# Kernel optimization log

Measured on AMD Instinct MI355X. Metric: run time of the kernel, lower is better.

The kernel has to match this reference:

```python
import jax, jax.numpy as jnp
import numpy as np

B, S, D = 2, 2048, 2048
H, KVH, HD = 16, 4, 128
E, TOPK, F = 8, 2, 1024
EPS = 1e-6
THETA = 10000.0


def _rmsnorm(x, w):
    return x * jax.lax.rsqrt(jnp.mean(x * x, axis=-1, keepdims=True) + EPS) * w


def _rope(x):
    # x: [B, S, h, HD]; positions 0..S-1 (prefill, pos offset 0)
    half = HD // 2
    inv_freq = THETA ** (-jnp.arange(half, dtype=jnp.float32) / half)  # [half]
    ang = jnp.arange(S, dtype=jnp.float32)[:, None] * inv_freq  # [S, half]
    cos = jnp.cos(ang)[None, :, None, :]
    sin = jnp.sin(ang)[None, :, None, :]
    x1, x2 = x[..., :half], x[..., half:]
    return jnp.concatenate([x1 * cos - x2 * sin, x1 * sin + x2 * cos], axis=-1)


def setup_inputs() -> dict:
    key = jax.random.key(0)
    ks = jax.random.split(key, 16)
    sc = 0.02
    return {
        "x": jax.random.normal(ks[0], (B, S, D), jnp.float32),
        "wattn_norm": 1.0 + 0.1 * jax.random.normal(ks[1], (D,), jnp.float32),
        "wq": sc * jax.random.normal(ks[2], (H * HD, D), jnp.float32),
        "wk": sc * jax.random.normal(ks[3], (KVH * HD, D), jnp.float32),
        "wv": sc * jax.random.normal(ks[4], (KVH * HD, D), jnp.float32),
        "wq_norm": 1.0 + 0.1 * jax.random.normal(ks[5], (HD,), jnp.float32),
        "wk_norm": 1.0 + 0.1 * jax.random.normal(ks[6], (HD,), jnp.float32),
        "wattn_out": sc * jax.random.normal(ks[7], (D, H * HD), jnp.float32),
        "wffn_norm": 1.0 + 0.1 * jax.random.normal(ks[8], (D,), jnp.float32),
        "w_router": sc * jax.random.normal(ks[9], (E, D), jnp.float32),
        "w_gate": sc * jax.random.normal(ks[10], (E, F, D), jnp.float32),
        "w_up": sc * jax.random.normal(ks[11], (E, F, D), jnp.float32),
        "w_down": sc * jax.random.normal(ks[12], (E, D, F), jnp.float32),
    }


def reference(x, wattn_norm, wq, wk, wv, wq_norm, wk_norm, wattn_out,
              wffn_norm, w_router, w_gate, w_up, w_down):
    # ---- attention sub-block ----
    h = _rmsnorm(x, wattn_norm)
    q = (h @ wq.T).reshape(B, S, H, HD)
    k = (h @ wk.T).reshape(B, S, KVH, HD)
    v = (h @ wv.T).reshape(B, S, KVH, HD)
    # per-head q/k rmsnorm (attn_q_norm / attn_k_norm)
    q = _rmsnorm(q, wq_norm)
    k = _rmsnorm(k, wk_norm)
    q = _rope(q)
    k = _rope(k)
    # GQA: repeat kv heads
    rep = H // KVH
    k = jnp.repeat(k, rep, axis=2)  # [B,S,H,HD]
    v = jnp.repeat(v, rep, axis=2)
    scores = jnp.einsum("bqhd,bkhd->bhqk", q, k) / np.sqrt(HD)
    causal = jnp.tril(jnp.ones((S, S), dtype=bool))
    scores = jnp.where(causal[None, None], scores, jnp.finfo(scores.dtype).min)
    attn = jax.nn.softmax(scores, axis=-1)
    o = jnp.einsum("bhqk,bkhd->bqhd", attn, v).reshape(B, S, H * HD)
    x = x + o @ wattn_out.T

    # ---- MoE FFN sub-block ----
    h = _rmsnorm(x, wffn_norm)  # [B,S,D]
    logits = h @ w_router.T  # [B,S,E]
    probs = jax.nn.softmax(logits, axis=-1)
    topv, topi = jax.lax.top_k(probs, TOPK)  # [B,S,K]
    topv = topv / jnp.sum(topv, axis=-1, keepdims=True)
    gates = jnp.sum(jax.nn.one_hot(topi, E, dtype=h.dtype) * topv[..., None], axis=-2)  # [B,S,E]

    t = h.reshape(B * S, D)
    g = gates.reshape(B * S, E)
    gh = jnp.einsum("td,efd->tef", t, w_gate)
    uh = jnp.einsum("td,efd->tef", t, w_up)
    act = jax.nn.silu(gh) * uh  # [T,E,F]
    eo = jnp.einsum("tef,edf->ted", act, w_down)  # [T,E,D]
    y = jnp.einsum("ted,te->td", eo, g).reshape(B, S, D)
    return x + y
```

## Files before the change

### kernel.cpp

```cpp
#include <hip/hip_runtime.h>

typedef _Float16 f16;
typedef __attribute__((ext_vector_type(8))) _Float16 f16x8;
typedef __attribute__((ext_vector_type(4))) _Float16 f16x4;
typedef __attribute__((ext_vector_type(4))) float f32x4;


#define GLD_LDS(gp, lp) \
  __builtin_amdgcn_global_load_lds((__attribute__((address_space(1))) void*)(gp), \
                                   (__attribute__((address_space(3))) void*)(lp), 16, 0, 0)


__global__ __launch_bounds__(256) void cvt_f16(const float* __restrict__ in,
                                               f16* __restrict__ outp, int n4) {
  int i = blockIdx.x * 256 + threadIdx.x;
  if (i >= n4) return;
  float4 v = ((const float4*)in)[i];
  f16x4 o;
  o[0] = (f16)v.x; o[1] = (f16)v.y; o[2] = (f16)v.z; o[3] = (f16)v.w;
  ((f16x4*)outp)[i] = o;
}

__global__ __launch_bounds__(256) void cvt_gu(const float* __restrict__ in,
                                              f16* __restrict__ outp, int up) {
  int i4 = blockIdx.x * 256 + threadIdx.x;
  int e = i4 >> 19;
  float4 v = ((const float4*)in)[i4];
  f16x4 o;
  o[0] = (f16)v.x; o[1] = (f16)v.y; o[2] = (f16)v.z; o[3] = (f16)v.w;
  ((f16x4*)outp)[i4 + (long)(e + up) * 524288] = o;
}

__global__ __launch_bounds__(256) void rope_tables(float* __restrict__ cost,
                                                   float* __restrict__ sint) {
  int i = blockIdx.x * 256 + threadIdx.x;
  if (i >= 2048 * 64) return;
  int s = i >> 6, j = i & 63;
  float invf = powf(10000.f, -(float)j * (1.f / 64.f));
  float ang = (float)s * invf;
  cost[i] = cosf(ang);
  sint[i] = sinf(ang);
}

__global__ __launch_bounds__(256) void rmsnorm_f16(const float* __restrict__ X,
                                                   const float* __restrict__ w,
                                                   f16* __restrict__ outp) {
  int t = blockIdx.x, tid = threadIdx.x;
  const float* row = X + (long)t * 2048;
  float4 v0 = ((const float4*)row)[tid];
  float4 v1 = ((const float4*)row)[tid + 256];
  float ss = v0.x * v0.x + v0.y * v0.y + v0.z * v0.z + v0.w * v0.w +
             v1.x * v1.x + v1.y * v1.y + v1.z * v1.z + v1.w * v1.w;
  for (int o = 32; o; o >>= 1) ss += __shfl_xor(ss, o);
  __shared__ float red[4];
  if ((tid & 63) == 0) red[tid >> 6] = ss;
  __syncthreads();
  ss = red[0] + red[1] + red[2] + red[3];
  float inv = rsqrtf(ss * (1.f / 2048.f) + 1e-6f);
  float4 w0 = ((const float4*)w)[tid];
  float4 w1 = ((const float4*)w)[tid + 256];
  f16x4 a, b;
  a[0] = (f16)(v0.x * inv * w0.x); a[1] = (f16)(v0.y * inv * w0.y);
  a[2] = (f16)(v0.z * inv * w0.z); a[3] = (f16)(v0.w * inv * w0.w);
  b[0] = (f16)(v1.x * inv * w1.x); b[1] = (f16)(v1.y * inv * w1.y);
  b[2] = (f16)(v1.z * inv * w1.z); b[3] = (f16)(v1.w * inv * w1.w);
  f16x4* orow = (f16x4*)(outp + (long)t * 2048);
  orow[tid] = a;
  orow[tid + 256] = b;
}

__global__ __launch_bounds__(256) void gemm_nt(
    const f16* __restrict__ A, const f16* __restrict__ W0,
    float* __restrict__ C, const float* __restrict__ Res, f16* __restrict__ Ct,
    f16* __restrict__ Ch,
    const int* __restrict__ gather, const int* __restrict__ eoff,
    const int* __restrict__ ecnt, int M, int N, int K, long wstride) {
  int e = blockIdx.z;
  int row0 = 0, nrows = M;
  if (eoff) { row0 = eoff[e]; nrows = ecnt[e]; }
  int mt = blockIdx.x;
  if (mt * 128 >= nrows) return;
  int nt = blockIdx.y;
  const f16* W = W0 + (long)e * wstride;

  __shared__ __align__(16) f16 As[128 * 64];
  __shared__ __align__(16) f16 Bs[128 * 64];

  int tid = threadIdx.x;
  int lane = tid & 63, wid = tid >> 6;
  int quad = lane >> 4, l15 = lane & 15;
  int wm = wid & 1, wn = wid >> 1;

  int srow = tid >> 3, ssub = tid & 7;
  long arowK[4], browK[4];
  for (int r = 0; r < 4; r++) {
    int rw = r * 32 + srow;
    int lr = mt * 128 + rw;
    int g = (lr < nrows) ? (row0 + lr) : row0;
    arowK[r] = (long)(gather ? gather[g] : g) * K;
    browK[r] = (long)(nt * 128 + rw) * K;
  }
  int gcol = ((ssub ^ (srow & 7)) * 8);

  f32x4 acc[4][4] = {};
  for (int k0 = 0; k0 < K; k0 += 64) {
    __syncthreads();
    for (int r = 0; r < 4; r++) {
      GLD_LDS(A + arowK[r] + k0 + gcol, &As[(r * 256 + tid) * 8]);
      GLD_LDS(W + browK[r] + k0 + gcol, &Bs[(r * 256 + tid) * 8]);
    }
    __syncthreads();
    for (int c = 0; c < 2; c++) {
      f16x8 av[4], bv[4];
      for (int i = 0; i < 4; i++) {
        int row = wm * 64 + i * 16 + l15;
        av[i] = *(const f16x8*)&As[row * 64 + (((c * 4 + quad) ^ (row & 7)) * 8)];
      }
      for (int j = 0; j < 4; j++) {
        int row = wn * 64 + j * 16 + l15;
        bv[j] = *(const f16x8*)&Bs[row * 64 + (((c * 4 + quad) ^ (row & 7)) * 8)];
      }
      for (int i = 0; i < 4; i++)
        for (int j = 0; j < 4; j++)
          acc[i][j] = __builtin_amdgcn_mfma_f32_16x16x32_f16(av[i], bv[j], acc[i][j], 0, 0, 0);
    }
  }
  for (int i = 0; i < 4; i++) {
    int lrb = mt * 128 + wm * 64 + i * 16 + quad * 4;
    for (int rr = 0; rr < 4; rr++) {
      int lr = lrb + rr;
      if (lr >= nrows) continue;
      long orow = row0 + lr;
      if (Ct) {
        int bb = (int)(orow >> 11), s2 = (int)(orow & 2047);
        for (int j = 0; j < 4; j++) {
          int col = nt * 128 + wn * 64 + j * 16 + l15;
          Ct[((long)(bb * N + col)) * 2048 + s2] = (f16)acc[i][j][rr];
        }
      } else if (Ch) {
        for (int j = 0; j < 4; j++) {
          int col = nt * 128 + wn * 64 + j * 16 + l15;
          Ch[orow * N + col] = (f16)acc[i][j][rr];
        }
      } else {
        for (int j = 0; j < 4; j++) {
          int col = nt * 128 + wn * 64 + j * 16 + l15;
          float v = acc[i][j][rr];
          if (Res) v += Res[orow * N + col];
          C[orow * N + col] = v;
        }
      }
    }
  }
}

__global__ __launch_bounds__(256) void qknorm_rope(
    const f16* __restrict__ X, const float* __restrict__ wn,
    const float* __restrict__ cost, const float* __restrict__ sint,
    f16* __restrict__ outp, int nh, float scale) {
  int t = blockIdx.x;
  int b = t >> 11, s = t & 2047;
  int wv = threadIdx.x >> 6, ln = threadIdx.x & 63;
  float c = cost[s * 64 + ln], sn = sint[s * 64 + ln];
  float w1 = wn[ln], w2 = wn[ln + 64];
  for (int h = wv; h < nh; h += 4) {
    const f16* row = X + ((long)t * nh + h) * 128;
    float x1 = (float)row[ln], x2 = (float)row[ln + 64];
    float ss = x1 * x1 + x2 * x2;
    for (int o = 32; o; o >>= 1) ss += __shfl_xor(ss, o);
    float inv = rsqrtf(ss * (1.f / 128.f) + 1e-6f);
    float n1 = x1 * inv * w1, n2 = x2 * inv * w2;
    f16* orow = outp + ((long)(b * nh + h) * 2048 + s) * 128;
    orow[ln] = (f16)((n1 * c - n2 * sn) * scale);
    orow[ln + 64] = (f16)((n1 * sn + n2 * c) * scale);
  }
}

__global__ __launch_bounds__(256, 3) void attn_kernel(
    const f16* __restrict__ Q, const f16* __restrict__ Kb,
    const f16* __restrict__ Vtg, f16* __restrict__ O) {
  int jj = blockIdx.x;
  int bh = blockIdx.y;
  int b = bh >> 4, h = bh & 15;
  int kvh = h >> 2;
  int tid = threadIdx.x, lane = tid & 63, wid = tid >> 6;
  int quad = lane >> 4, l15 = lane & 15;

  const f16* Kg = Kb + (long)(b * 4 + kvh) * 2048 * 128;
  const f16* Vg = Vtg + (long)(b * 4 + kvh) * 128 * 2048;

  const int KSTR = 136, VSTR = 72, PSTR = 72;
  __shared__ __align__(16) f16 Ks[64 * 136];
  __shared__ __align__(16) f16 Vs[128 * 72];
  __shared__ __align__(16) f16 Ps[4][16 * 72];

  int krow[4], kc[4], vd[4], vc[4];
  for (int c2 = 0; c2 < 4; c2++) {
    int idx = c2 * 256 + tid;
    krow[c2] = idx >> 4; kc[c2] = (idx & 15) * 8;
    vd[c2] = idx >> 3;  vc[c2] = (idx & 7) * 8;
  }

  for (int ph = 0; ph < 2; ph++) {
    int qt = ph ? (31 - jj) : jj;
    int q0 = qt * 64;
    int rowb = q0 + wid * 16 + quad * 4;

    const f16* Qb = Q + ((long)(b * 16 + h) * 2048 + q0 + wid * 16) * 128;
    f16x8 qfr[4];
    for (int c = 0; c < 4; c++)
      qfr[c] = *(const f16x8*)(Qb + (long)l15 * 128 + c * 32 + quad * 8);

    f32x4 oacc[8] = {};
    float li[4] = {0.f, 0.f, 0.f, 0.f};

    f16x8 kpre[4], vpre[4];
    for (int c2 = 0; c2 < 4; c2++) {
      kpre[c2] = *(const f16x8*)(Kg + (long)krow[c2] * 128 + kc[c2]);
      vpre[c2] = *(const f16x8*)(Vg + (long)vd[c2] * 2048 + vc[c2]);
    }

    for (int kt = 0; kt <= qt; kt++) {
      int k0 = kt * 64;
      __syncthreads();
      for (int c2 = 0; c2 < 4; c2++) {
        *(f16x8*)&Ks[krow[c2] * KSTR + kc[c2]] = kpre[c2];
        *(f16x8*)&Vs[vd[c2] * VSTR + vc[c2]] = vpre[c2];
      }
      if (kt < qt) {
        int k1 = (kt + 1) * 64;
        for (int c2 = 0; c2 < 4; c2++) {
          kpre[c2] = *(const f16x8*)(Kg + (long)(k1 + krow[c2]) * 128 + kc[c2]);
          vpre[c2] = *(const f16x8*)(Vg + (long)vd[c2] * 2048 + k1 + vc[c2]);
        }
      }
      __syncthreads();
      f32x4 sc[4] = {};
      for (int hf = 0; hf < 4; hf++)
        for (int c = 0; c < 4; c++) {
          f16x8 kf = *(const f16x8*)&Ks[(hf * 16 + l15) * KSTR + c * 32 + quad * 8];
          sc[hf] = __builtin_amdgcn_mfma_f32_16x16x32_f16(qfr[c], kf, sc[hf], 0, 0, 0);
        }
      bool dg = (kt == qt);
      for (int r = 0; r < 4; r++) {
        int row = rowb + r;
        float acc = 0.f;
        for (int hf = 0; hf < 4; hf++) {
          float pv = exp2f(sc[hf][r] * 1.44269504f - 7.21347520f);
          if (dg && (k0 + hf * 16 + l15 > row)) pv = 0.f;
          f16 phh = (f16)pv;
          Ps[wid][(quad * 4 + r) * PSTR + hf * 16 + l15] = phh;
          acc += (float)phh;
        }
        li[r] += acc;
      }
      for (int c = 0; c < 2; c++) {
        f16x8 pa = *(const f16x8*)&Ps[wid][l15 * PSTR + c * 32 + quad * 8];
        for (int n = 0; n < 8; n++) {
          f16x8 vf = *(const f16x8*)&Vs[(n * 16 + l15) * VSTR + c * 32 + quad * 8];
          oacc[n] = __builtin_amdgcn_mfma_f32_16x16x32_f16(pa, vf, oacc[n], 0, 0, 0);
        }
      }
    }
    for (int r = 0; r < 4; r++) {
      float s = li[r];
      for (int o = 8; o; o >>= 1) s += __shfl_xor(s, o);
      float inv = 1.f / s;
      int row = rowb + r;
      long basep = ((long)(b * 2048 + row)) * 2048 + h * 128;
      for (int n = 0; n < 8; n++)
        O[basep + n * 16 + l15] = (f16)(oacc[n][r] * inv);
    }
  }
}

__global__ void zero8(int* p) { if (threadIdx.x < 8) p[threadIdx.x] = 0; }

__global__ __launch_bounds__(256) void router_kernel(
    const float* __restrict__ X2, const float* __restrict__ wfn,
    const float* __restrict__ wr, int* __restrict__ route,
    int* __restrict__ toke, float* __restrict__ tokw) {
  int t = blockIdx.x, tid = threadIdx.x;
  const float* row = X2 + (long)t * 2048;
  float xv[8];
  float ss = 0.f;
  for (int j = 0; j < 8; j++) {
    float v = row[tid + j * 256];
    xv[j] = v;
    ss += v * v;
  }
  for (int o = 32; o; o >>= 1) ss += __shfl_xor(ss, o);
  __shared__ float red[4];
  int lane = tid & 63, wid = tid >> 6;
  if (lane == 0) red[wid] = ss;
  __syncthreads();
  ss = red[0] + red[1] + red[2] + red[3];
  float inv = rsqrtf(ss * (1.f / 2048.f) + 1e-6f);
  float xw[8];
  for (int j = 0; j < 8; j++) xw[j] = xv[j] * wfn[tid + j * 256];
  float lg[8];
  for (int e = 0; e < 8; e++) {
    float a = 0.f;
    for (int j = 0; j < 8; j++) a += xw[j] * wr[e * 2048 + tid + j * 256];
    for (int o = 32; o; o >>= 1) a += __shfl_xor(a, o);
    lg[e] = a;
  }
  __shared__ float lred[4][8];
  if (lane == 0)
    for (int e = 0; e < 8; e++) lred[wid][e] = lg[e];
  __syncthreads();
  if (tid == 0) {
    float l[8];
    for (int e = 0; e < 8; e++)
      l[e] = (lred[0][e] + lred[1][e] + lred[2][e] + lred[3][e]) * inv;
    int i0 = 0; float b0 = l[0];
    for (int e = 1; e < 8; e++) if (l[e] > b0) { b0 = l[e]; i0 = e; }
    int i1 = -1; float b1 = -__builtin_inff();
    for (int e = 0; e < 8; e++) {
      if (e == i0) continue;
      if (l[e] > b1) { b1 = l[e]; i1 = e; }
    }
    float w0 = 1.f / (1.f + expf(b1 - b0));
    toke[t * 2] = i0; toke[t * 2 + 1] = i1;
    tokw[t * 2] = w0; tokw[t * 2 + 1] = 1.f - w0;
    atomicAdd(&route[i0], 1);
    atomicAdd(&route[i1], 1);
  }
}

__global__ void prefix_kernel(int* route) {
  if (threadIdx.x == 0) {
    int o = 0;
    for (int e = 0; e < 8; e++) { route[16 + e] = o; o += route[e]; }
  }
  if (threadIdx.x < 8) route[8 + threadIdx.x] = 0;
}

__global__ __launch_bounds__(256) void scatter_kernel(
    const int* __restrict__ toke, const float* __restrict__ tokw,
    int* __restrict__ route, int* __restrict__ tokc,
    float* __restrict__ gatew, int* __restrict__ tslots) {
  int t = blockIdx.x * 256 + threadIdx.x;
  if (t >= 4096) return;
  for (int j = 0; j < 2; j++) {
    int e = toke[t * 2 + j];
    int p = atomicAdd(&route[8 + e], 1);
    int slot = route[16 + e] + p;
    tokc[slot] = t;
    gatew[slot] = tokw[t * 2 + j];
    tslots[t * 2 + j] = slot;
  }
}

__global__ __launch_bounds__(256) void moe_act(const f16* __restrict__ gu,
                                               const float* __restrict__ gatew,
                                               f16* __restrict__ act) {
  int i8 = blockIdx.x * 256 + threadIdx.x;
  int slot = i8 >> 7, f8 = (i8 & 127) * 8;
  const f16* rowp = gu + (long)slot * 2048;
  f16x8 g8 = *(const f16x8*)(rowp + f8);
  f16x8 u8 = *(const f16x8*)(rowp + 1024 + f8);
  float gw = gatew[slot];
  f16x8 o;
  for (int j = 0; j < 8; j++) {
    float g = (float)g8[j], u = (float)u8[j];
    o[j] = (f16)(gw * g * u / (1.f + expf(-g)));
  }
  *(f16x8*)(act + (long)slot * 1024 + f8) = o;
}

__global__ __launch_bounds__(256) void final_add(float* __restrict__ outp,
                                                 const f16* __restrict__ eo,
                                                 const int* __restrict__ tslots) {
  int i4 = blockIdx.x * 256 + threadIdx.x;
  int t = i4 >> 9, d4 = (i4 & 511) * 4;
  int s0 = tslots[t * 2], s1 = tslots[t * 2 + 1];
  float4 a = ((const float4*)outp)[i4];
  f16x4 e0 = *(const f16x4*)(eo + (long)s0 * 2048 + d4);
  f16x4 e1 = *(const f16x4*)(eo + (long)s1 * 2048 + d4);
  a.x += (float)e0[0] + (float)e1[0];
  a.y += (float)e0[1] + (float)e1[1];
  a.z += (float)e0[2] + (float)e1[2];
  a.w += (float)e0[3] + (float)e1[3];
  ((float4*)outp)[i4] = a;
}


extern "C" void kernel_launch(void* const* d_in, const int* in_sizes, int n_in,
                              void* d_out, int out_size, void* d_ws, size_t ws_size,
                              hipStream_t stream) {
  const float* x   = (const float*)d_in[0];
  const float* wan = (const float*)d_in[1];
  const float* wq  = (const float*)d_in[2];
  const float* wk  = (const float*)d_in[3];
  const float* wvp = (const float*)d_in[4];
  const float* wqn = (const float*)d_in[5];
  const float* wkn = (const float*)d_in[6];
  const float* wo  = (const float*)d_in[7];
  const float* wfn = (const float*)d_in[8];
  const float* wr  = (const float*)d_in[9];
  const float* wg  = (const float*)d_in[10];
  const float* wu  = (const float*)d_in[11];
  const float* wd  = (const float*)d_in[12];
  float* out = (float*)d_out;
  char* ws = (char*)d_ws;

  size_t off = 0;
  auto alloc = [&](size_t b) { size_t r = off; off += (b + 255) & ~(size_t)255; return r; };
  size_t o_RA  = alloc((size_t)16 * 1024 * 1024);
  size_t o_RB  = alloc((size_t)16 * 1024 * 1024);
  size_t o_RC  = alloc((size_t)16 * 1024 * 1024);
  size_t o_kp  = alloc((size_t)4 * 1024 * 1024);
  size_t o_kh  = alloc((size_t)4 * 1024 * 1024);
  size_t o_vt  = alloc((size_t)4 * 1024 * 1024);
  size_t o_gf  = alloc((size_t)32 * 1024 * 1024);
  size_t o_wqh = alloc((size_t)2048 * 2048 * 2);
  size_t o_wkh = alloc((size_t)512 * 2048 * 2);
  size_t o_wvh = alloc((size_t)512 * 2048 * 2);
  size_t o_woh = alloc((size_t)2048 * 2048 * 2);
  size_t o_wgu = alloc((size_t)8 * 2048 * 2048 * 2);
  size_t o_wdh = alloc((size_t)8 * 2048 * 1024 * 2);
  size_t o_cos = alloc((size_t)2048 * 64 * 4);
  size_t o_sin = alloc((size_t)2048 * 64 * 4);
  size_t o_rt  = alloc(256);
  size_t o_toke = alloc(4096 * 2 * 4);
  size_t o_tokw = alloc(4096 * 2 * 4);
  size_t o_tokc = alloc(4096 * 2 * 4);
  size_t o_gw   = alloc(4096 * 2 * 4);
  size_t o_ts   = alloc(4096 * 2 * 4);
  (void)ws_size; (void)in_sizes; (void)n_in; (void)out_size;

  f16* h16   = (f16*)(ws + o_RA);
  f16* oh    = (f16*)(ws + o_RA);
  f16* act16 = (f16*)(ws + o_RA);
  f16* qpre  = (f16*)(ws + o_RB);
  f16* h2h   = (f16*)(ws + o_RB);
  f16* qh    = (f16*)(ws + o_RC);
  f16* kpre  = (f16*)(ws + o_kp);
  f16* kh    = (f16*)(ws + o_kh);
  f16* vth   = (f16*)(ws + o_vt);
  f16* gf16  = (f16*)(ws + o_gf);
  f16* eo16  = (f16*)(ws + o_gf);
  f16* wqh = (f16*)(ws + o_wqh);
  f16* wkh = (f16*)(ws + o_wkh);
  f16* wvh = (f16*)(ws + o_wvh);
  f16* woh = (f16*)(ws + o_woh);
  f16* wguh = (f16*)(ws + o_wgu);
  f16* wdh = (f16*)(ws + o_wdh);
  float* cost = (float*)(ws + o_cos);
  float* sint = (float*)(ws + o_sin);
  int* route = (int*)(ws + o_rt);
  int* toke = (int*)(ws + o_toke);
  float* tokw = (float*)(ws + o_tokw);
  int* tokc = (int*)(ws + o_tokc);
  float* gatew = (float*)(ws + o_gw);
  int* tslots = (int*)(ws + o_ts);

  cvt_f16<<<4096, 256, 0, stream>>>(wq, wqh, 1048576);
  cvt_f16<<<1024, 256, 0, stream>>>(wk, wkh, 262144);
  cvt_f16<<<1024, 256, 0, stream>>>(wvp, wvh, 262144);
  cvt_f16<<<4096, 256, 0, stream>>>(wo, woh, 1048576);
  cvt_gu<<<16384, 256, 0, stream>>>(wg, wguh, 0);
  cvt_gu<<<16384, 256, 0, stream>>>(wu, wguh, 1);
  cvt_f16<<<16384, 256, 0, stream>>>(wd, wdh, 4194304);
  rope_tables<<<512, 256, 0, stream>>>(cost, sint);

  rmsnorm_f16<<<4096, 256, 0, stream>>>(x, wan, h16);
  gemm_nt<<<dim3(32, 16, 1), 256, 0, stream>>>(h16, wqh, nullptr, nullptr, nullptr, qpre, nullptr, nullptr, nullptr, 4096, 2048, 2048, 0);
  gemm_nt<<<dim3(32, 4, 1), 256, 0, stream>>>(h16, wkh, nullptr, nullptr, nullptr, kpre, nullptr, nullptr, nullptr, 4096, 512, 2048, 0);
  gemm_nt<<<dim3(32, 4, 1), 256, 0, stream>>>(h16, wvh, nullptr, nullptr, vth, nullptr, nullptr, nullptr, nullptr, 4096, 512, 2048, 0);
  qknorm_rope<<<4096, 256, 0, stream>>>(qpre, wqn, cost, sint, qh, 16, 0.08838834764831845f);
  qknorm_rope<<<4096, 256, 0, stream>>>(kpre, wkn, cost, sint, kh, 4, 1.0f);
  attn_kernel<<<dim3(16, 32, 1), 256, 0, stream>>>(qh, kh, vth, oh);
  gemm_nt<<<dim3(32, 16, 1), 256, 0, stream>>>(oh, woh, out, x, nullptr, nullptr, nullptr, nullptr, nullptr, 4096, 2048, 2048, 0);

  rmsnorm_f16<<<4096, 256, 0, stream>>>(out, wfn, h2h);
  zero8<<<1, 64, 0, stream>>>(route);
  router_kernel<<<4096, 256, 0, stream>>>(out, wfn, wr, route, toke, tokw);
  prefix_kernel<<<1, 64, 0, stream>>>(route);
  scatter_kernel<<<16, 256, 0, stream>>>(toke, tokw, route, tokc, gatew, tslots);
  gemm_nt<<<dim3(16, 16, 8), 256, 0, stream>>>(h2h, wguh, nullptr, nullptr, nullptr, gf16, tokc, route + 16, route, 4096, 2048, 2048, 4194304);
  moe_act<<<4096, 256, 0, stream>>>(gf16, gatew, act16);
  gemm_nt<<<dim3(16, 16, 8), 256, 0, stream>>>(act16, wdh, nullptr, nullptr, nullptr, eo16, nullptr, route + 16, route, 4096, 2048, 1024, 2097152);
  final_add<<<8192, 256, 0, stream>>>(out, eo16, tslots);
}
```

Measured before the change: 1.094 ms.

## Fuse QKV projection GEMMs and add XCD-aware block swizzle

Concatenates the Q, K and V weight matrices so the three projections run as one GEMM, with an epilogue that writes Q, K and transposed V to separate buffers. Adds a block-index remap that groups consecutive tiles onto the same XCD for L2 reuse. Doubles the M-tile count of the MoE expert GEMMs so experts with more than 2048 routed rows are fully covered. This cuts launch overhead and underfilled K/V launches, at the cost of many early-exit blocks in the MoE grids.

Result: faster. 994.3 us (-9.1%).

```diff
diff --git a/kernel.cpp b/kernel.cpp
--- a/kernel.cpp
+++ b/kernel.cpp
@@ -73,14 +73,18 @@
     const f16* __restrict__ A, const f16* __restrict__ W0,
     float* __restrict__ C, const float* __restrict__ Res, f16* __restrict__ Ct,
     f16* __restrict__ Ch,
+    f16* __restrict__ Cq, f16* __restrict__ Ck, f16* __restrict__ Cv,
     const int* __restrict__ gather, const int* __restrict__ eoff,
     const int* __restrict__ ecnt, int M, int N, int K, long wstride) {
   int e = blockIdx.z;
   int row0 = 0, nrows = M;
   if (eoff) { row0 = eoff[e]; nrows = ecnt[e]; }
-  int mt = blockIdx.x;
+  int gx = gridDim.x;
+  int T = gx * gridDim.y;
+  int lin = blockIdx.x + blockIdx.y * gx;
+  if ((T & 7) == 0) lin = (lin & 7) * (T >> 3) + (lin >> 3);
+  int mt = lin % gx, nt = lin / gx;
   if (mt * 128 >= nrows) return;
-  int nt = blockIdx.y;
   const f16* W = W0 + (long)e * wstride;
 
   __shared__ __align__(16) f16 As[128 * 64];
@@ -131,7 +135,20 @@
       int lr = lrb + rr;
       if (lr >= nrows) continue;
       long orow = row0 + lr;
-      if (Ct) {
+      if (Cq) {
+        int bb = (int)(orow >> 11), s2 = (int)(orow & 2047);
+        for (int j = 0; j < 4; j++) {
+          int col = nt * 128 + wn * 64 + j * 16 + l15;
+          f16 v = (f16)acc[i][j][rr];
+          if (col < 2048) Cq[orow * 2048 + col] = v;
+          else if (col < 2560) Ck[orow * 512 + (col - 2048)] = v;
+          else {
+            int cc = col - 2560;
+            int kv = cc >> 7, d = cc & 127;
+            Cv[((long)((bb * 4 + kv) * 128 + d)) * 2048 + s2] = v;
+          }
+        }
+      } else if (Ct) {
         int bb = (int)(orow >> 11), s2 = (int)(orow & 2047);
         for (int j = 0; j < 4; j++) {
           int col = nt * 128 + wn * 64 + j * 16 + l15;
@@ -414,9 +431,7 @@
   size_t o_kh  = alloc((size_t)4 * 1024 * 1024);
   size_t o_vt  = alloc((size_t)4 * 1024 * 1024);
   size_t o_gf  = alloc((size_t)32 * 1024 * 1024);
-  size_t o_wqh = alloc((size_t)2048 * 2048 * 2);
-  size_t o_wkh = alloc((size_t)512 * 2048 * 2);
-  size_t o_wvh = alloc((size_t)512 * 2048 * 2);
+  size_t o_wqkv = alloc((size_t)3072 * 2048 * 2);
   size_t o_woh = alloc((size_t)2048 * 2048 * 2);
   size_t o_wgu = alloc((size_t)8 * 2048 * 2048 * 2);
   size_t o_wdh = alloc((size_t)8 * 2048 * 1024 * 2);
@@ -441,9 +456,7 @@
   f16* vth   = (f16*)(ws + o_vt);
   f16* gf16  = (f16*)(ws + o_gf);
   f16* eo16  = (f16*)(ws + o_gf);
-  f16* wqh = (f16*)(ws + o_wqh);
-  f16* wkh = (f16*)(ws + o_wkh);
-  f16* wvh = (f16*)(ws + o_wvh);
+  f16* wqkvh = (f16*)(ws + o_wqkv);
   f16* woh = (f16*)(ws + o_woh);
   f16* wguh = (f16*)(ws + o_wgu);
   f16* wdh = (f16*)(ws + o_wdh);
@@ -456,9 +469,9 @@
   float* gatew = (float*)(ws + o_gw);
   int* tslots = (int*)(ws + o_ts);
 
-  cvt_f16<<<4096, 256, 0, stream>>>(wq, wqh, 1048576);
-  cvt_f16<<<1024, 256, 0, stream>>>(wk, wkh, 262144);
-  cvt_f16<<<1024, 256, 0, stream>>>(wvp, wvh, 262144);
+  cvt_f16<<<4096, 256, 0, stream>>>(wq, wqkvh, 1048576);
+  cvt_f16<<<1024, 256, 0, stream>>>(wk, wqkvh + (size_t)2048 * 2048, 262144);
+  cvt_f16<<<1024, 256, 0, stream>>>(wvp, wqkvh + (size_t)2560 * 2048, 262144);
   cvt_f16<<<4096, 256, 0, stream>>>(wo, woh, 1048576);
   cvt_gu<<<16384, 256, 0, stream>>>(wg, wguh, 0);
   cvt_gu<<<16384, 256, 0, stream>>>(wu, wguh, 1);
@@ -466,21 +479,19 @@
   rope_tables<<<512, 256, 0, stream>>>(cost, sint);
 
   rmsnorm_f16<<<4096, 256, 0, stream>>>(x, wan, h16);
-  gemm_nt<<<dim3(32, 16, 1), 256, 0, stream>>>(h16, wqh, nullptr, nullptr, nullptr, qpre, nullptr, nullptr, nullptr, 4096, 2048, 2048, 0);
-  gemm_nt<<<dim3(32, 4, 1), 256, 0, stream>>>(h16, wkh, nullptr, nullptr, nullptr, kpre, nullptr, nullptr, nullptr, 4096, 512, 2048, 0);
-  gemm_nt<<<dim3(32, 4, 1), 256, 0, stream>>>(h16, wvh, nullptr, nullptr, vth, nullptr, nullptr, nullptr, nullptr, 4096, 512, 2048, 0);
+  gemm_nt<<<dim3(32, 24, 1), 256, 0, stream>>>(h16, wqkvh, nullptr, nullptr, nullptr, nullptr, qpre, kpre, vth, nullptr, nullptr, nullptr, 4096, 3072, 2048, 0);
   qknorm_rope<<<4096, 256, 0, stream>>>(qpre, wqn, cost, sint, qh, 16, 0.08838834764831845f);
   qknorm_rope<<<4096, 256, 0, stream>>>(kpre, wkn, cost, sint, kh, 4, 1.0f);
   attn_kernel<<<dim3(16, 32, 1), 256, 0, stream>>>(qh, kh, vth, oh);
-  gemm_nt<<<dim3(32, 16, 1), 256, 0, stream>>>(oh, woh, out, x, nullptr, nullptr, nullptr, nullptr, nullptr, 4096, 2048, 2048, 0);
+  gemm_nt<<<dim3(32, 16, 1), 256, 0, stream>>>(oh, woh, out, x, nullptr, nullptr, nullptr, nullptr, nullptr, nullptr, nullptr, nullptr, 4096, 2048, 2048, 0);
 
   rmsnorm_f16<<<4096, 256, 0, stream>>>(out, wfn, h2h);
   zero8<<<1, 64, 0, stream>>>(route);
   router_kernel<<<4096, 256, 0, stream>>>(out, wfn, wr, route, toke, tokw);
   prefix_kernel<<<1, 64, 0, stream>>>(route);
   scatter_kernel<<<16, 256, 0, stream>>>(toke, tokw, route, tokc, gatew, tslots);
-  gemm_nt<<<dim3(16, 16, 8), 256, 0, stream>>>(h2h, wguh, nullptr, nullptr, nullptr, gf16, tokc, route + 16, route, 4096, 2048, 2048, 4194304);
+  gemm_nt<<<dim3(32, 16, 8), 256, 0, stream>>>(h2h, wguh, nullptr, nullptr, nullptr, gf16, nullptr, nullptr, nullptr, tokc, route + 16, route, 4096, 2048, 2048, 4194304);
   moe_act<<<4096, 256, 0, stream>>>(gf16, gatew, act16);
-  gemm_nt<<<dim3(16, 16, 8), 256, 0, stream>>>(act16, wdh, nullptr, nullptr, nullptr, eo16, nullptr, route + 16, route, 4096, 2048, 1024, 2097152);
+  gemm_nt<<<dim3(32, 16, 8), 256, 0, stream>>>(act16, wdh, nullptr, nullptr, nullptr, eo16, nullptr, nullptr, nullptr, nullptr, route + 16, route, 4096, 2048, 1024, 2097152);
   final_add<<<8192, 256, 0, stream>>>(out, eo16, tslots);
 }
```
